# Kernel tuning notes

Measured on AMD Instinct MI355X. Metric: run time of the kernel, lower is better.

## Reference

```python
import jax, jax.numpy as jnp
import numpy as np

DIM, INNER, NH = 256, 64, 8
HD = INNER // NH  # 8
B, H, W = 2, 48, 48
EPS = 1e-6


def _ln2d(x, w, b):
    # channel-first LayerNorm over dim=1, biased variance (matches LayerNorm2d)
    u = x.mean(axis=1, keepdims=True)
    s = ((x - u) ** 2).mean(axis=1, keepdims=True)
    xn = (x - u) / jnp.sqrt(s + EPS)
    return w[None, :, None, None] * xn + b[None, :, None, None]


def _conv1x1(x, w, b):
    return jnp.einsum('oc,bchw->bohw', w, x) + b[None, :, None, None]


def _attn(q, k, v):
    # q,k,v: [B, INNER, H, W] -> global attention over HW tokens per head
    Bq, C, Hh, Ww = q.shape
    split = lambda t: t.reshape(Bq, NH, HD, Hh * Ww)
    q, k, v = split(q), split(k), split(v)
    scale = HD ** -0.5
    attn = jnp.einsum('bhdn,bhdm->bhnm', q, k) * scale  # [B,nh,HW,HW]
    attn = jax.nn.softmax(attn, axis=-1)
    out = jnp.einsum('bhnm,bhdm->bhdn', attn, v)
    return out.reshape(Bq, C, Hh, Ww)


def setup_inputs() -> dict:
    key = jax.random.key(0)
    ks = jax.random.split(key, 12)
    w = lambda k, o, i: jax.random.normal(k, (o, i), dtype=jnp.float32) * 0.02
    d = {
        'f_rgb': jax.random.normal(ks[0], (B, DIM, H, W), dtype=jnp.float32),
        'f_ir': jax.random.normal(ks[1], (B, DIM, H, W), dtype=jnp.float32),
        'nr_w': jnp.ones(DIM), 'nr_b': jnp.zeros(DIM),
        'ni_w': jnp.ones(DIM), 'ni_b': jnp.zeros(DIM),
        'qr_w': w(ks[2], INNER, DIM), 'qr_b': jnp.zeros(INNER),
        'kvi_w': w(ks[3], 2 * INNER, DIM), 'kvi_b': jnp.zeros(2 * INNER),
        'qi_w': w(ks[4], INNER, DIM), 'qi_b': jnp.zeros(INNER),
        'kvr_w': w(ks[5], 2 * INNER, DIM), 'kvr_b': jnp.zeros(2 * INNER),
        'pr_w': w(ks[6], DIM, INNER), 'pr_b': jnp.zeros(DIM),
        'pr_lnw': jnp.ones(DIM), 'pr_lnb': jnp.zeros(DIM),
        'pi_w': w(ks[7], DIM, INNER), 'pi_b': jnp.zeros(DIM),
        'pi_lnw': jnp.ones(DIM), 'pi_lnb': jnp.zeros(DIM),
        'gr_w': w(ks[8], DIM, 2 * DIM), 'gr_b': jnp.zeros(DIM),
        'gi_w': w(ks[9], DIM, 2 * DIM), 'gi_b': jnp.zeros(DIM),
    }
    return d


def reference(f_rgb, f_ir, nr_w, nr_b, ni_w, ni_b, qr_w, qr_b, kvi_w, kvi_b,
              qi_w, qi_b, kvr_w, kvr_b, pr_w, pr_b, pr_lnw, pr_lnb,
              pi_w, pi_b, pi_lnw, pi_lnb, gr_w, gr_b, gi_w, gi_b):
    n_rgb = _ln2d(f_rgb, nr_w, nr_b)
    n_ir = _ln2d(f_ir, ni_w, ni_b)

    # RGB queries attend to IR keys/values
    q_r = _conv1x1(n_rgb, qr_w, qr_b)
    kv_i = _conv1x1(n_ir, kvi_w, kvi_b)
    k_i, v_i = kv_i[:, :INNER], kv_i[:, INNER:]
    rgb_cross = _attn(q_r, k_i, v_i)
    rgb_cross = _ln2d(_conv1x1(rgb_cross, pr_w, pr_b), pr_lnw, pr_lnb)
    gate_r = jax.nn.sigmoid(_conv1x1(jnp.concatenate([f_rgb, rgb_cross], axis=1), gr_w, gr_b))
    f_rgb_out = f_rgb + gate_r * rgb_cross

    # IR queries attend to RGB keys/values
    q_i = _conv1x1(n_ir, qi_w, qi_b)
    kv_r = _conv1x1(n_rgb, kvr_w, kvr_b)
    k_r, v_r = kv_r[:, :INNER], kv_r[:, INNER:]
    ir_cross = _attn(q_i, k_r, v_r)
    ir_cross = _ln2d(_conv1x1(ir_cross, pi_w, pi_b), pi_lnw, pi_lnb)
    gate_i = jax.nn.sigmoid(_conv1x1(jnp.concatenate([f_ir, ir_cross], axis=1), gi_w, gi_b))
    f_ir_out = f_ir + gate_i * ir_cross

    return (f_rgb_out, f_ir_out)
```

## Files before the change

### kernel.cpp

```cpp
#include <hip/hip_runtime.h>

static constexpr int kDim   = 256;
static constexpr int kInner = 64;
static constexpr int kNH    = 8;
static constexpr int kB     = 2;
static constexpr int kP     = 2304;
static constexpr float kScale = 0.35355339059327373f;
static constexpr float kEps   = 1e-6f;

typedef __fp16   fp16x2 __attribute__((ext_vector_type(2)));
typedef _Float16 half4f __attribute__((ext_vector_type(4)));
typedef _Float16 half8  __attribute__((ext_vector_type(8)));
typedef float    f32x4  __attribute__((ext_vector_type(4)));

static constexpr size_t oXq  = 0;
static constexpr size_t oQ16 = 2359296;
static constexpr size_t oK16 = 2949120;
static constexpr size_t oV16 = 3538944;
static constexpr size_t oA16 = 4128768;
static constexpr size_t oC16 = 4718592;
static constexpr size_t oW16 = 7077888;
static constexpr size_t kInpStride = 294912;

__global__ __launch_bounds__(256) void prep(
    const float* __restrict__ x0, const float* __restrict__ w0,
    const float* __restrict__ b0, const float* __restrict__ x1,
    const float* __restrict__ w1, const float* __restrict__ b1,
    _Float16* __restrict__ Xq,
    const float* __restrict__ qr_w, const float* __restrict__ kvr_w,
    const float* __restrict__ qi_w, const float* __restrict__ kvi_w,
    const float* __restrict__ pr_w, const float* __restrict__ pi_w,
    const float* __restrict__ gr_w, const float* __restrict__ gi_w,
    _Float16* __restrict__ w16)
{
    if (blockIdx.x >= 576) {
        const int flat = blockIdx.x - 576;
        const int y = flat >> 6, x = flat & 63;
        const float* src; _Float16* dst; int n;
        _Float16* Aq = w16;
        _Float16* Ap = w16 + 98304;
        _Float16* Ag = w16 + 131072;
        switch (y) {
            case 0: src = qr_w;  dst = Aq;          n = 16384;  break;
            case 1: src = kvr_w; dst = Aq + 16384;  n = 32768;  break;
            case 2: src = qi_w;  dst = Aq + 49152;  n = 16384;  break;
            case 3: src = kvi_w; dst = Aq + 65536;  n = 32768;  break;
            case 4: src = pr_w;  dst = Ap;          n = 16384;  break;
            case 5: src = pi_w;  dst = Ap + 16384;  n = 16384;  break;
            case 6: src = gr_w;  dst = Ag;          n = 131072; break;
            default:src = gi_w;  dst = Ag + 131072; n = 131072; break;
        }
        for (int i = x * 256 + threadIdx.x; i < n; i += 64 * 256)
            dst[i] = (_Float16)src[i];
        return;
    }
    __shared__ float sb[16][16];
    __shared__ float ssb[16][16];
    const int fid = blockIdx.x;
    const int xcd = fid & 7, q = fid >> 3;
    const int inp = (xcd >> 2) & 1, bb = (xcd >> 1) & 1, half = xcd & 1;
    const float* x = inp ? x1 : x0;
    const float* w = inp ? w1 : w0;
    const float* b = inp ? b1 : b0;
    const int pos = threadIdx.x & 15;
    const int grp = threadIdx.x >> 4;
    const int p   = half * 1152 + q * 16 + pos;
    const size_t base = (size_t)bb * kDim * kP + p;
    const int c0 = grp * 16;

    float v[16];
    float s = 0.f, ss = 0.f;
    #pragma unroll
    for (int j = 0; j < 16; ++j) {
        v[j] = x[base + (size_t)(c0 + j) * kP];
        s += v[j]; ss += v[j] * v[j];
    }
    sb[grp][pos] = s; ssb[grp][pos] = ss;
    __syncthreads();
    float st = 0.f, sst = 0.f;
    #pragma unroll
    for (int g = 0; g < 16; ++g) { st += sb[g][pos]; sst += ssb[g][pos]; }
    const float mean = st * (1.f / kDim);
    const float rstd = rsqrtf(sst * (1.f / kDim) - mean * mean + kEps);
    half8 h0, h1;
    #pragma unroll
    for (int j = 0; j < 8; ++j) {
        h0[j] = (_Float16)((v[j]     - mean) * rstd * w[c0 + j]     + b[c0 + j]);
        h1[j] = (_Float16)((v[j + 8] - mean) * rstd * w[c0 + j + 8] + b[c0 + j + 8]);
    }
    _Float16* dst = Xq + ((size_t)(inp * 2 + bb) * kP + p) * 256 + c0;
    *(half8*)dst       = h0;
    *(half8*)(dst + 8) = h1;
}

__global__ __launch_bounds__(256) void ln_post(
    const _Float16* __restrict__ c16,
    const float* __restrict__ w0, const float* __restrict__ b0,
    const float* __restrict__ w1, const float* __restrict__ b1,
    const float* __restrict__ f0, const float* __restrict__ f1,
    _Float16* __restrict__ Xg)
{
    __shared__ float sb[16][16];
    __shared__ float ssb[16][16];
    const int fid = blockIdx.x;
    const int xcd = fid & 7, q = fid >> 3;
    const int s = (xcd >> 2) & 1, bb = (xcd >> 1) & 1, half = xcd & 1;
    const float* w = s ? w1 : w0;
    const float* b = s ? b1 : b0;
    const float* F = s ? f1 : f0;
    const int pos = threadIdx.x & 15;
    const int grp = threadIdx.x >> 4;
    const int p   = half * 1152 + q * 16 + pos;
    const int c0  = grp * 16;
    const size_t combo = s * 2 + bb;

    const _Float16* cp = c16 + (combo * kP + p) * 256 + c0;
    const half8 g0 = *(const half8*)cp;
    const half8 g1 = *(const half8*)(cp + 8);
    float v[16];
    float sm = 0.f, ssq = 0.f;
    #pragma unroll
    for (int j = 0; j < 8; ++j) {
        v[j] = (float)g0[j]; v[j + 8] = (float)g1[j];
    }
    #pragma unroll
    for (int j = 0; j < 16; ++j) { sm += v[j]; ssq += v[j] * v[j]; }
    sb[grp][pos] = sm; ssb[grp][pos] = ssq;
    __syncthreads();
    float st = 0.f, sst = 0.f;
    #pragma unroll
    for (int g = 0; g < 16; ++g) { st += sb[g][pos]; sst += ssb[g][pos]; }
    const float mean = st * (1.f / kDim);
    const float rstd = rsqrtf(sst * (1.f / kDim) - mean * mean + kEps);

    _Float16* xrow = Xg + (combo * kP + p) * 512;
    half8 o0, o1;
    #pragma unroll
    for (int j = 0; j < 8; ++j) {
        o0[j] = (_Float16)((v[j]     - mean) * rstd * w[c0 + j]     + b[c0 + j]);
        o1[j] = (_Float16)((v[j + 8] - mean) * rstd * w[c0 + j + 8] + b[c0 + j + 8]);
    }
    *(half8*)(xrow + 256 + c0)     = o0;
    *(half8*)(xrow + 256 + c0 + 8) = o1;
    const size_t fbase = (size_t)bb * kDim * kP + p;
    half8 r0, r1;
    #pragma unroll
    for (int j = 0; j < 8; ++j) {
        r0[j] = (_Float16)F[fbase + (size_t)(c0 + j) * kP];
        r1[j] = (_Float16)F[fbase + (size_t)(c0 + j + 8) * kP];
    }
    *(half8*)(xrow + c0)     = r0;
    *(half8*)(xrow + c0 + 8) = r1;
}

template <int M, int K, int EPI>
__global__ __launch_bounds__(256) void gemm_f16(
    const _Float16* __restrict__ A,
    const _Float16* __restrict__ B,
    const float* __restrict__ b0, const float* __restrict__ b1,
    const float* __restrict__ b2, const float* __restrict__ b3,
    _Float16* __restrict__ o16a, _Float16* __restrict__ o16b, _Float16* __restrict__ o16c,
    const float* __restrict__ f0, const float* __restrict__ f1,
    float* __restrict__ outp)
{
    constexpr int MT64 = M / 64;
    const int fid = blockIdx.x;
    const int xcd = fid & 7, q = fid >> 3;
    const int s = (xcd >> 2) & 1, bb = (xcd >> 1) & 1, half = xcd & 1;
    const int ot64 = (q % MT64) * 64;
    const int pt   = q / MT64;
    const int wv = threadIdx.x >> 6, lane = threadIdx.x & 63;
    const int r16 = lane & 15, g = lane >> 4;
    const int ot = ot64 + wv * 16;
    const int p0 = half * 1152 + pt * 64;
    const int combo = s * 2 + bb;

    const _Float16* Ar = A + ((size_t)s * M + ot + r16) * K + 8 * g;
    const _Float16* Br = B + ((size_t)combo * kP + p0 + r16) * K + 8 * g;
    f32x4 acc0[4], acc1[4];
    #pragma unroll
    for (int ps = 0; ps < 4; ++ps) {
        acc0[ps] = (f32x4){0.f, 0.f, 0.f, 0.f};
        acc1[ps] = (f32x4){0.f, 0.f, 0.f, 0.f};
    }
    #pragma unroll 4
    for (int c0 = 0; c0 < K; c0 += 32) {
        const half8 a8 = *(const half8*)(Ar + c0);
        half8 b8[4];
        #pragma unroll
        for (int ps = 0; ps < 4; ++ps)
            b8[ps] = *(const half8*)(Br + (size_t)(16 * ps) * K + c0);
        const half4f al = {a8[0], a8[1], a8[2], a8[3]};
        const half4f ah = {a8[4], a8[5], a8[6], a8[7]};
        #pragma unroll
        for (int ps = 0; ps < 4; ++ps) {
            const half4f bl = {b8[ps][0], b8[ps][1], b8[ps][2], b8[ps][3]};
            const half4f bh = {b8[ps][4], b8[ps][5], b8[ps][6], b8[ps][7]};
            acc0[ps] = __builtin_amdgcn_mfma_f32_16x16x16f16(al, bl, acc0[ps], 0, 0, 0);
            acc1[ps] = __builtin_amdgcn_mfma_f32_16x16x16f16(ah, bh, acc1[ps], 0, 0, 0);
        }
    }
    const int obase = ot + 4 * g;

    #pragma unroll
    for (int ps = 0; ps < 4; ++ps) {
        float acc[4];
        #pragma unroll
        for (int i = 0; i < 4; ++i) acc[i] = acc0[ps][i] + acc1[ps][i];
        const int p = p0 + 16 * ps + r16;

        if constexpr (EPI == 0) {
            const int dlo = 4 * (g & 1);
            if (ot < 64) {
                const float* qb = s ? b1 : b0;
                const float4 bv = *(const float4*)(qb + obase);
                const int h = (ot >> 3) + (g >> 1);
                half4f o = { (_Float16)((acc[0] + bv.x) * kScale), (_Float16)((acc[1] + bv.y) * kScale),
                             (_Float16)((acc[2] + bv.z) * kScale), (_Float16)((acc[3] + bv.w) * kScale) };
                *(half4f*)(o16a + (((size_t)combo * 8 + h) * kP + p) * 8 + dlo) = o;
            } else if (ot < 128) {
                const float* kb = s ? b3 : b2;
                const float4 bv = *(const float4*)(kb + obase - 64);
                const int h = ((ot - 64) >> 3) + (g >> 1);
                half4f o = { (_Float16)(acc[0] + bv.x), (_Float16)(acc[1] + bv.y),
                             (_Float16)(acc[2] + bv.z), (_Float16)(acc[3] + bv.w) };
                *(half4f*)(o16b + (((size_t)combo * 8 + h) * kP + p) * 8 + dlo) = o;
            } else {
                const float* kb = s ? b3 : b2;
                const float4 bv = *(const float4*)(kb + obase - 64);
                const int h = ((ot - 128) >> 3) + (g >> 1);
                const float* bvp = (const float*)&bv;
                #pragma unroll
                for (int i = 0; i < 4; ++i)
                    o16c[(((size_t)combo * 8 + h) * 8 + dlo + i) * kP + p] = (_Float16)(acc[i] + bvp[i]);
            }
        } else if constexpr (EPI == 1) {
            const float* pb = s ? b1 : b0;
            const float4 bv = *(const float4*)(pb + obase);
            half4f o = { (_Float16)(acc[0] + bv.x), (_Float16)(acc[1] + bv.y),
                         (_Float16)(acc[2] + bv.z), (_Float16)(acc[3] + bv.w) };
            *(half4f*)(o16a + ((size_t)combo * kP + p) * 256 + obase) = o;
        } else {
            const float* gb = s ? b1 : b0;
            const float4 bv = *(const float4*)(gb + obase);
            const float* bvp = (const float*)&bv;
            const half4f cx = *(const half4f*)(B + ((size_t)combo * kP + p) * 512 + 256 + obase);
            const float* F = s ? f1 : f0;
            #pragma unroll
            for (int i = 0; i < 4; ++i) {
                const int o = obase + i;
                const float gt = 1.f / (1.f + __expf(-(acc[i] + bvp[i])));
                const float fb = F[((size_t)bb * kDim + o) * kP + p];
                outp[((size_t)combo * kDim + o) * kP + p] = fb + gt * (float)cx[i];
            }
        }
    }
}

__global__ __launch_bounds__(256) void attn_mfma(
    const _Float16* __restrict__ q16, const _Float16* __restrict__ k16,
    const _Float16* __restrict__ vt16, _Float16* __restrict__ a16)
{
    __shared__ _Float16 Ksm[16 * 64 * 4];
    __shared__ _Float16 Vsm[16 * 66 * 4];
    const int st = blockIdx.z;
    const _Float16* Qg = q16  + (size_t)st * kInpStride;
    const _Float16* Kg = k16  + (size_t)(1 - st) * kInpStride;
    const _Float16* Vg = vt16 + (size_t)(1 - st) * kInpStride;
    const int bh = blockIdx.y;
    const int bb = bh >> 3, h = bh & 7;
    const int tid  = threadIdx.x;
    const int wv   = tid >> 6;
    const int lane = tid & 63;
    const int r16  = lane & 15;
    const int g    = lane >> 4;

    #pragma unroll
    for (int j = 0; j < 2; ++j) {
        const int s = tid + 256 * j;
        const int kt = s >> 5, m = s & 31;
        *(half4f*)(Ksm + (kt * 64 + 32 + m) * 4) = (half4f){0, 0, 0, 0};
        const int rv = 8 + (m & 7), gv = m >> 3;
        const half4f vv = (rv == 8)
            ? (half4f){(_Float16)1.f, (_Float16)1.f, (_Float16)1.f, (_Float16)1.f}
            : (half4f){0, 0, 0, 0};
        *(half4f*)(Vsm + (kt * 66 + gv * 16 + rv) * 4) = vv;
    }

    const int qg = blockIdx.x * 64 + wv * 16 + r16;
    half4f qf = (half4f){0, 0, 0, 0};
    if (g < 2) qf = *(const half4f*)(Qg + ((size_t)bh * kP + qg) * 8 + g * 4);

    const int vd = tid >> 5, vc8 = (tid & 31) * 8;
    const int vkt = vc8 >> 4, vgv = (vc8 & 15) >> 2;
    _Float16* kdst = Ksm + ((tid >> 4) * 64 + (tid & 15)) * 4;
    _Float16* vdst = Vsm + (vkt * 66 + vgv * 16 + vd) * 4;
    const _Float16* ksrc = Kg + ((size_t)bh * kP + tid) * 8;
    const _Float16* vsrc = Vg + (size_t)(bh * 8 + vd) * kP + vc8;

    half8 kreg = *(const half8*)ksrc;
    half8 vreg = *(const half8*)vsrc;

    f32x4 of = (f32x4){0.f, 0.f, 0.f, 0.f};

    for (int ch = 0; ch < 9; ++ch) {
        if (ch) __syncthreads();
        *(half4f*)kdst        = (half4f){kreg[0], kreg[1], kreg[2], kreg[3]};
        *(half4f*)(kdst + 64) = (half4f){kreg[4], kreg[5], kreg[6], kreg[7]};
        *(half4f*)vdst        = (half4f){vreg[0], vreg[1], vreg[2], vreg[3]};
        *(half4f*)(vdst + 64) = (half4f){vreg[4], vreg[5], vreg[6], vreg[7]};
        __syncthreads();
        if (ch < 8) {
            kreg = *(const half8*)(ksrc + (size_t)(ch + 1) * 2048);
            vreg = *(const half8*)(vsrc + (size_t)(ch + 1) * 256);
        }
        #pragma unroll
        for (int kt = 0; kt < 16; ++kt) {
            const half4f kf = *(const half4f*)(Ksm + (kt * 64 + lane) * 4);
            f32x4 sv = __builtin_amdgcn_mfma_f32_16x16x16f16(kf, qf, (f32x4){0.f,0.f,0.f,0.f}, 0, 0, 0);
            const float e0 = __expf(sv[0]), e1 = __expf(sv[1]);
            const float e2 = __expf(sv[2]), e3 = __expf(sv[3]);
            const fp16x2 lo = __builtin_amdgcn_cvt_pkrtz(e0, e1);
            const fp16x2 hi = __builtin_amdgcn_cvt_pkrtz(e2, e3);
            const half4f pf = { (_Float16)lo[0], (_Float16)lo[1],
                                (_Float16)hi[0], (_Float16)hi[1] };
            const half4f vf = *(const half4f*)(Vsm + (kt * 66 + lane) * 4);
            of = __builtin_amdgcn_mfma_f32_16x16x16f16(vf, pf, of, 0, 0, 0);
        }
    }
    const float rsv = __shfl(of[0], 32 + r16, 64);
    const float inv = 1.f / rsv;
    if (g < 2) {
        half4f o = { (_Float16)(of[0] * inv), (_Float16)(of[1] * inv),
                     (_Float16)(of[2] * inv), (_Float16)(of[3] * inv) };
        *(half4f*)(a16 + ((size_t)(st * 2 + bb) * kP + qg) * 64 + h * 8 + g * 4) = o;
    }
}

extern "C" void kernel_launch(void* const* d_in, const int* in_sizes, int n_in,
                              void* d_out, int out_size, void* d_ws, size_t ws_size,
                              hipStream_t stream)
{
    const float* f_rgb  = (const float*)d_in[0];
    const float* f_ir   = (const float*)d_in[1];
    const float* nr_w   = (const float*)d_in[2];
    const float* nr_b   = (const float*)d_in[3];
    const float* ni_w   = (const float*)d_in[4];
    const float* ni_b   = (const float*)d_in[5];
    const float* qr_w   = (const float*)d_in[6];
    const float* qr_b   = (const float*)d_in[7];
    const float* kvi_w  = (const float*)d_in[8];
    const float* kvi_b  = (const float*)d_in[9];
    const float* qi_w   = (const float*)d_in[10];
    const float* qi_b   = (const float*)d_in[11];
    const float* kvr_w  = (const float*)d_in[12];
    const float* kvr_b  = (const float*)d_in[13];
    const float* pr_w   = (const float*)d_in[14];
    const float* pr_b   = (const float*)d_in[15];
    const float* pr_lnw = (const float*)d_in[16];
    const float* pr_lnb = (const float*)d_in[17];
    const float* pi_w   = (const float*)d_in[18];
    const float* pi_b   = (const float*)d_in[19];
    const float* pi_lnw = (const float*)d_in[20];
    const float* pi_lnb = (const float*)d_in[21];
    const float* gr_w   = (const float*)d_in[22];
    const float* gr_b   = (const float*)d_in[23];
    const float* gi_w   = (const float*)d_in[24];
    const float* gi_b   = (const float*)d_in[25];

    _Float16* hb   = (_Float16*)d_ws;
    _Float16* Xq   = hb + oXq;
    _Float16* q16  = hb + oQ16;
    _Float16* k16  = hb + oK16;
    _Float16* vt16 = hb + oV16;
    _Float16* a16  = hb + oA16;
    _Float16* Xg   = hb;
    _Float16* c16  = hb + oC16;
    _Float16* W16  = hb + oW16;
    _Float16* Aq   = W16;
    _Float16* Ap   = W16 + 98304;
    _Float16* Ag   = W16 + 131072;

    float* outp = (float*)d_out;
    const dim3 blk(256);

    prep<<<dim3(1088), blk, 0, stream>>>(f_rgb, nr_w, nr_b, f_ir, ni_w, ni_b, Xq,
                                         qr_w, kvr_w, qi_w, kvi_w, pr_w, pi_w, gr_w, gi_w, W16);
    gemm_f16<192, 256, 0><<<dim3(432), blk, 0, stream>>>(
        Aq, Xq, qr_b, qi_b, kvr_b, kvi_b, q16, k16, vt16, nullptr, nullptr, nullptr);
    attn_mfma<<<dim3(36, 16, 2), blk, 0, stream>>>(q16, k16, vt16, a16);
    gemm_f16<256, 64, 1><<<dim3(576), blk, 0, stream>>>(
        Ap, a16, pr_b, pi_b, nullptr, nullptr, c16, nullptr, nullptr, nullptr, nullptr, nullptr);
    ln_post<<<dim3(576), blk, 0, stream>>>(c16, pr_lnw, pr_lnb, pi_lnw, pi_lnb,
                                           f_rgb, f_ir, Xg);
    gemm_f16<256, 512, 2><<<dim3(576), blk, 0, stream>>>(
        Ag, Xg, gr_b, gi_b, nullptr, nullptr, nullptr, nullptr, nullptr, f_rgb, f_ir, outp);
}
```

Baseline: 104.3 us.

## Fuse output projection GEMM with post LayerNorm; split attention accumulator chain

Replaces the separate projection GEMM and the LayerNorm/pack kernel with one proj_ln kernel. It computes the 64->256 projection via MFMA in registers, reduces LN statistics across waves in shared memory, and writes the gate input rows directly, so the c16 intermediate round trip and one launch go away. Separately, the attention PV accumulation now alternates between two accumulators to shorten the MFMA dependency chain. The fused kernel loads weights directly from global memory with no LDS staging, which may cost some reuse.

```diff
diff --git a/kernel.cpp b/kernel.cpp
--- a/kernel.cpp
+++ b/kernel.cpp
@@ -18,7 +18,6 @@
 static constexpr size_t oK16 = 2949120;
 static constexpr size_t oV16 = 3538944;
 static constexpr size_t oA16 = 4128768;
-static constexpr size_t oC16 = 4718592;
 static constexpr size_t oW16 = 7077888;
 static constexpr size_t kInpStride = 294912;
 
@@ -93,66 +92,6 @@
     *(half8*)(dst + 8) = h1;
 }
 
-__global__ __launch_bounds__(256) void ln_post(
-    const _Float16* __restrict__ c16,
-    const float* __restrict__ w0, const float* __restrict__ b0,
-    const float* __restrict__ w1, const float* __restrict__ b1,
-    const float* __restrict__ f0, const float* __restrict__ f1,
-    _Float16* __restrict__ Xg)
-{
-    __shared__ float sb[16][16];
-    __shared__ float ssb[16][16];
-    const int fid = blockIdx.x;
-    const int xcd = fid & 7, q = fid >> 3;
-    const int s = (xcd >> 2) & 1, bb = (xcd >> 1) & 1, half = xcd & 1;
-    const float* w = s ? w1 : w0;
-    const float* b = s ? b1 : b0;
-    const float* F = s ? f1 : f0;
-    const int pos = threadIdx.x & 15;
-    const int grp = threadIdx.x >> 4;
-    const int p   = half * 1152 + q * 16 + pos;
-    const int c0  = grp * 16;
-    const size_t combo = s * 2 + bb;
-
-    const _Float16* cp = c16 + (combo * kP + p) * 256 + c0;
-    const half8 g0 = *(const half8*)cp;
-    const half8 g1 = *(const half8*)(cp + 8);
-    float v[16];
-    float sm = 0.f, ssq = 0.f;
-    #pragma unroll
-    for (int j = 0; j < 8; ++j) {
-        v[j] = (float)g0[j]; v[j + 8] = (float)g1[j];
-    }
-    #pragma unroll
-    for (int j = 0; j < 16; ++j) { sm += v[j]; ssq += v[j] * v[j]; }
-    sb[grp][pos] = sm; ssb[grp][pos] = ssq;
-    __syncthreads();
-    float st = 0.f, sst = 0.f;
-    #pragma unroll
-    for (int g = 0; g < 16; ++g) { st += sb[g][pos]; sst += ssb[g][pos]; }
-    const float mean = st * (1.f / kDim);
-    const float rstd = rsqrtf(sst * (1.f / kDim) - mean * mean + kEps);
-
-    _Float16* xrow = Xg + (combo * kP + p) * 512;
-    half8 o0, o1;
-    #pragma unroll
-    for (int j = 0; j < 8; ++j) {
-        o0[j] = (_Float16)((v[j]     - mean) * rstd * w[c0 + j]     + b[c0 + j]);
-        o1[j] = (_Float16)((v[j + 8] - mean) * rstd * w[c0 + j + 8] + b[c0 + j + 8]);
-    }
-    *(half8*)(xrow + 256 + c0)     = o0;
-    *(half8*)(xrow + 256 + c0 + 8) = o1;
-    const size_t fbase = (size_t)bb * kDim * kP + p;
-    half8 r0, r1;
-    #pragma unroll
-    for (int j = 0; j < 8; ++j) {
-        r0[j] = (_Float16)F[fbase + (size_t)(c0 + j) * kP];
-        r1[j] = (_Float16)F[fbase + (size_t)(c0 + j + 8) * kP];
-    }
-    *(half8*)(xrow + c0)     = r0;
-    *(half8*)(xrow + c0 + 8) = r1;
-}
-
 template <int M, int K, int EPI>
 __global__ __launch_bounds__(256) void gemm_f16(
     const _Float16* __restrict__ A,
@@ -234,12 +173,6 @@
                 for (int i = 0; i < 4; ++i)
                     o16c[(((size_t)combo * 8 + h) * 8 + dlo + i) * kP + p] = (_Float16)(acc[i] + bvp[i]);
             }
-        } else if constexpr (EPI == 1) {
-            const float* pb = s ? b1 : b0;
-            const float4 bv = *(const float4*)(pb + obase);
-            half4f o = { (_Float16)(acc[0] + bv.x), (_Float16)(acc[1] + bv.y),
-                         (_Float16)(acc[2] + bv.z), (_Float16)(acc[3] + bv.w) };
-            *(half4f*)(o16a + ((size_t)combo * kP + p) * 256 + obase) = o;
         } else {
             const float* gb = s ? b1 : b0;
             const float4 bv = *(const float4*)(gb + obase);
@@ -254,6 +187,92 @@
                 outp[((size_t)combo * kDim + o) * kP + p] = fb + gt * (float)cx[i];
             }
         }
+    }
+}
+
+__global__ __launch_bounds__(256) void proj_ln(
+    const _Float16* __restrict__ a16, const _Float16* __restrict__ Ap,
+    const float* __restrict__ pb0, const float* __restrict__ pb1,
+    const float* __restrict__ w0, const float* __restrict__ b0,
+    const float* __restrict__ w1, const float* __restrict__ b1,
+    const float* __restrict__ f0, const float* __restrict__ f1,
+    _Float16* __restrict__ Xg)
+{
+    __shared__ float sb[4][4][16];
+    __shared__ float ssb[4][4][16];
+    const int fid = blockIdx.x;
+    const int xcd = fid & 7, q = fid >> 3;
+    const int s = (xcd >> 2) & 1, bb = (xcd >> 1) & 1, half = xcd & 1;
+    const int wv = threadIdx.x >> 6, lane = threadIdx.x & 63;
+    const int r16 = lane & 15, g = lane >> 4;
+    const int p = half * 1152 + q * 16 + r16;
+    const int combo = s * 2 + bb;
+    const float* pb = s ? pb1 : pb0;
+    const float* w  = s ? w1 : w0;
+    const float* b  = s ? b1 : b0;
+    const float* F  = s ? f1 : f0;
+
+    const _Float16* Br = a16 + ((size_t)combo * kP + p) * 64 + 8 * g;
+    const half8 bA = *(const half8*)Br;
+    const half8 bB = *(const half8*)(Br + 32);
+    const half4f bl0 = {bA[0], bA[1], bA[2], bA[3]};
+    const half4f bh0 = {bA[4], bA[5], bA[6], bA[7]};
+    const half4f bl1 = {bB[0], bB[1], bB[2], bB[3]};
+    const half4f bh1 = {bB[4], bB[5], bB[6], bB[7]};
+
+    float cval[4][4];
+    float psum = 0.f, psq = 0.f;
+    #pragma unroll
+    for (int t = 0; t < 4; ++t) {
+        const int ot = wv * 64 + t * 16;
+        const _Float16* Ar = Ap + ((size_t)s * 256 + ot + r16) * 64 + 8 * g;
+        const half8 aA = *(const half8*)Ar;
+        const half8 aB = *(const half8*)(Ar + 32);
+        const half4f al0 = {aA[0], aA[1], aA[2], aA[3]};
+        const half4f ah0 = {aA[4], aA[5], aA[6], aA[7]};
+        const half4f al1 = {aB[0], aB[1], aB[2], aB[3]};
+        const half4f ah1 = {aB[4], aB[5], aB[6], aB[7]};
+        f32x4 acc0 = __builtin_amdgcn_mfma_f32_16x16x16f16(al0, bl0, (f32x4){0.f,0.f,0.f,0.f}, 0, 0, 0);
+        acc0 = __builtin_amdgcn_mfma_f32_16x16x16f16(al1, bl1, acc0, 0, 0, 0);
+        f32x4 acc1 = __builtin_amdgcn_mfma_f32_16x16x16f16(ah0, bh0, (f32x4){0.f,0.f,0.f,0.f}, 0, 0, 0);
+        acc1 = __builtin_amdgcn_mfma_f32_16x16x16f16(ah1, bh1, acc1, 0, 0, 0);
+        const float4 bv = *(const float4*)(pb + ot + 4 * g);
+        const float* bvp = (const float*)&bv;
+        #pragma unroll
+        for (int i = 0; i < 4; ++i) {
+            const float v = acc0[i] + acc1[i] + bvp[i];
+            cval[t][i] = v;
+            psum += v; psq += v * v;
+        }
+    }
+    sb[wv][g][r16] = psum; ssb[wv][g][r16] = psq;
+    __syncthreads();
+    float st = 0.f, sst = 0.f;
+    #pragma unroll
+    for (int w2 = 0; w2 < 4; ++w2)
+        #pragma unroll
+        for (int g2 = 0; g2 < 4; ++g2) { st += sb[w2][g2][r16]; sst += ssb[w2][g2][r16]; }
+    const float mean = st * (1.f / kDim);
+    const float rstd = rsqrtf(sst * (1.f / kDim) - mean * mean + kEps);
+
+    _Float16* xrow = Xg + ((size_t)combo * kP + p) * 512;
+    #pragma unroll
+    for (int t = 0; t < 4; ++t) {
+        const int o4 = wv * 64 + t * 16 + 4 * g;
+        const float4 lw = *(const float4*)(w + o4);
+        const float4 lb = *(const float4*)(b + o4);
+        const float* lwp = (const float*)&lw;
+        const float* lbp = (const float*)&lb;
+        half4f o;
+        #pragma unroll
+        for (int i = 0; i < 4; ++i)
+            o[i] = (_Float16)((cval[t][i] - mean) * rstd * lwp[i] + lbp[i]);
+        *(half4f*)(xrow + 256 + o4) = o;
+        half4f r;
+        #pragma unroll
+        for (int i = 0; i < 4; ++i)
+            r[i] = (_Float16)F[((size_t)bb * kDim + o4 + i) * kP + p];
+        *(half4f*)(xrow + o4) = r;
     }
 }
 
@@ -301,7 +320,8 @@
     half8 kreg = *(const half8*)ksrc;
     half8 vreg = *(const half8*)vsrc;
 
-    f32x4 of = (f32x4){0.f, 0.f, 0.f, 0.f};
+    f32x4 of0 = (f32x4){0.f, 0.f, 0.f, 0.f};
+    f32x4 of1 = (f32x4){0.f, 0.f, 0.f, 0.f};
 
     for (int ch = 0; ch < 9; ++ch) {
         if (ch) __syncthreads();
@@ -325,9 +345,11 @@
             const half4f pf = { (_Float16)lo[0], (_Float16)lo[1],
                                 (_Float16)hi[0], (_Float16)hi[1] };
             const half4f vf = *(const half4f*)(Vsm + (kt * 66 + lane) * 4);
-            of = __builtin_amdgcn_mfma_f32_16x16x16f16(vf, pf, of, 0, 0, 0);
-        }
-    }
+            if (kt & 1) of1 = __builtin_amdgcn_mfma_f32_16x16x16f16(vf, pf, of1, 0, 0, 0);
+            else        of0 = __builtin_amdgcn_mfma_f32_16x16x16f16(vf, pf, of0, 0, 0, 0);
+        }
+    }
+    const f32x4 of = of0 + of1;
     const float rsv = __shfl(of[0], 32 + r16, 64);
     const float inv = 1.f / rsv;
     if (g < 2) {
@@ -375,7 +397,6 @@
     _Float16* vt16 = hb + oV16;
     _Float16* a16  = hb + oA16;
     _Float16* Xg   = hb;
-    _Float16* c16  = hb + oC16;
     _Float16* W16  = hb + oW16;
     _Float16* Aq   = W16;
     _Float16* Ap   = W16 + 98304;
@@ -389,9 +410,8 @@
     gemm_f16<192, 256, 0><<<dim3(432), blk, 0, stream>>>(
         Aq, Xq, qr_b, qi_b, kvr_b, kvi_b, q16, k16, vt16, nullptr, nullptr, nullptr);
     attn_mfma<<<dim3(36, 16, 2), blk, 0, stream>>>(q16, k16, vt16, a16);
-    gemm_f16<256, 64, 1><<<dim3(576), blk, 0, stream>>>(
-        Ap, a16, pr_b, pi_b, nullptr, nullptr, c16, nullptr, nullptr, nullptr, nullptr, nullptr);
-    ln_post<<<dim3(576), blk, 0, stream>>>(c16, pr_lnw, pr_lnb, pi_lnw, pi_lnb,
+    proj_ln<<<dim3(576), blk, 0, stream>>>(a16, Ap, pr_b, pi_b,
+                                           pr_lnw, pr_lnb, pi_lnw, pi_lnb,
                                            f_rgb, f_ir, Xg);
     gemm_f16<256, 512, 2><<<dim3(576), blk, 0, stream>>>(
         Ag, Xg, gr_b, gi_b, nullptr, nullptr, nullptr, nullptr, nullptr, f_rgb, f_ir, outp);
```

New measurement: 101.8 us. -2.4%, faster.
